# Optimization experiments

Hardware: AMD Instinct MI355X
Metric: run time of the kernel (lower is better)

The kernel has to match this reference:

```python
import jax, jax.numpy as jnp
import numpy as np

B, N, D, K, DSPACE, NFREQ = 4, 4096, 256, 16, 3, 5
BN_EPS = 1e-5


def setup_inputs() -> dict:
    key = jax.random.key(0)
    ks = jax.random.split(key, 12)
    s = 1.0 / np.sqrt(D)
    pe_in = DSPACE * 2 * NFREQ + DSPACE  # 33
    return {
        "xyz": jax.random.normal(ks[0], (B, N, DSPACE), jnp.float32),
        "feats": jax.random.normal(ks[1], (B, N, D), jnp.float32),
        "w_q": jax.random.uniform(ks[2], (D, D), jnp.float32, -s, s),
        "w_k": jax.random.uniform(ks[3], (D, D), jnp.float32, -s, s),
        "w_v": jax.random.uniform(ks[4], (D, D), jnp.float32, -s, s),
        "g_w1": jax.random.uniform(ks[5], (D, D), jnp.float32, -s, s),
        "g_b1": jax.random.uniform(ks[6], (D,), jnp.float32, -s, s),
        "g_w2": jax.random.uniform(ks[7], (D, D), jnp.float32, -s, s),
        "g_b2": jax.random.uniform(ks[8], (D,), jnp.float32, -s, s),
        "pe_w": jax.random.uniform(ks[9], (D, pe_in), jnp.float32, -s, s),
        "pe_b": jax.random.uniform(ks[10], (D,), jnp.float32, -s, s),
        "bn_w": jnp.ones((D,), jnp.float32),
        "bn_b": jnp.zeros((D,), jnp.float32),
    }


def _gather_knn(points, idx):
    # points [b,n,c], idx [b,n,k] -> [b,n,k,c]
    return jax.vmap(lambda p, i: p[i])(points, idx)


def reference(xyz, feats, w_q, w_k, w_v, g_w1, g_b1, g_w2, g_b2, pe_w, pe_b, bn_w, bn_b):
    # KNN (no grad in original): full pairwise sq-distance + top-k smallest
    dists = jnp.sum((xyz[:, :, None] - xyz[:, None]) ** 2, axis=-1)  # [b,n,n]
    _, knn_idx = jax.lax.top_k(-dists, K)  # [b,n,k], ascending distance
    knn_idx = jax.lax.stop_gradient(knn_idx)
    knn_xyz = jax.lax.stop_gradient(_gather_knn(xyz, knn_idx))  # [b,n,k,3]

    q = feats @ w_q.T                               # [b,n,d]
    k_g = _gather_knn(feats @ w_k.T, knn_idx)       # [b,n,k,d]
    v_g = _gather_knn(feats @ w_v.T, knn_idx)       # [b,n,k,d]

    pos_diff = xyz[:, :, None] - knn_xyz            # [b,n,k,3]
    freqs = jnp.linspace(1.0, 2.0 ** NFREQ, NFREQ).astype(pos_diff.dtype)
    embeds = [pos_diff]
    for f in freqs:
        embeds.append(jnp.sin(pos_diff * f))
        embeds.append(jnp.cos(pos_diff * f))
    pos_embed = jnp.concatenate(embeds, axis=-1)    # [b,n,k,33]
    pos_encode = pos_embed @ pe_w.T + pe_b          # [b,n,k,d]

    edges = q[:, :, None] - k_g + pos_encode        # [b,n,k,d]
    h = jax.nn.relu(edges @ g_w1.T + g_b1)
    attn = h @ g_w2.T + g_b2                        # [b,n,k,d]
    attn = jax.nn.softmax(attn, axis=-2)            # softmax over neighbors

    res = jnp.einsum('bnkf,bnkf->bnf', attn, v_g + pos_encode) + feats

    # BatchNorm1d over channel dim, training-mode batch stats (biased var)
    mean = jnp.mean(res, axis=(0, 1))
    var = jnp.var(res, axis=(0, 1))
    res = (res - mean) * jax.lax.rsqrt(var + BN_EPS) * bn_w + bn_b
    return res
```

## Files before the change

kernel.cpp:

```cpp
#include <hip/hip_runtime.h>

#define BB 4
#define NN 4096
#define DD 256
#define KK 16
#define PTS 2
#define SA 280
#define SE 104
#define SK 264

typedef __bf16 bf16;
typedef __attribute__((ext_vector_type(8))) __bf16 bf16x8;
typedef __attribute__((ext_vector_type(4))) __bf16 bf16x4;
typedef __attribute__((ext_vector_type(4))) float f32x4;

__global__ __launch_bounds__(256) void prep_kernel(
    const float* __restrict__ wq, const float* __restrict__ wk,
    const float* __restrict__ wv, const float* __restrict__ w1,
    const float* __restrict__ w2, const float* __restrict__ pw,
    bf16* __restrict__ wqb, bf16* __restrict__ wkb, bf16* __restrict__ wvb,
    bf16* __restrict__ w1b, bf16* __restrict__ w2b, bf16* __restrict__ pwb,
    float* __restrict__ sums) {
  const int idx = blockIdx.x * 256 + threadIdx.x;
  wqb[idx] = (bf16)wq[idx];
  wkb[idx] = (bf16)wk[idx];
  wvb[idx] = (bf16)wv[idx];
  w1b[idx] = (bf16)w1[idx];
  w2b[idx] = (bf16)w2[idx];
  if (idx < 256 * 64) {
    const int n = idx >> 6, c = idx & 63;
    pwb[idx] = (c < 33) ? (bf16)pw[n * 33 + c] : (bf16)0.f;
  }
  if (idx < 2 * DD) sums[idx] = 0.f;
}

__global__ __launch_bounds__(256, 2) void knn_v3(const float* __restrict__ xyz,
                                                 int* __restrict__ knn) {
  const int lane = threadIdx.x & 63;
  const int wv = threadIdx.x >> 6;
  const int row = blockIdx.x * 4 + wv;
  const int b = row >> 12, i = row & (NN - 1);
  const float* xb = xyz + (size_t)b * NN * 3;
  const float xi = xb[i * 3 + 0], yi = xb[i * 3 + 1], zi = xb[i * 3 + 2];
  unsigned long long cand[64];
#pragma unroll
  for (int c = 0; c < 64; ++c) {
    const int j = c * 64 + lane;
    const float dx = xi - xb[j * 3 + 0];
    const float dy = yi - xb[j * 3 + 1];
    const float dz = zi - xb[j * 3 + 2];
    const float d = dx * dx + dy * dy + dz * dz;
    const unsigned long long fb = (unsigned long long)(__float_as_uint(d)) + 1ull;
    cand[c] = (fb << 32) | (unsigned int)j;
  }
  unsigned long long gm[8];
#pragma unroll
  for (int g = 0; g < 8; ++g) {
    unsigned long long mn = cand[g * 8];
#pragma unroll
    for (int s = 1; s < 8; ++s)
      if (cand[g * 8 + s] < mn) mn = cand[g * 8 + s];
    gm[g] = mn;
  }
  unsigned int myj = 0u;
  for (int r = 0; r < KK; ++r) {
    unsigned long long lmin = gm[0];
#pragma unroll
    for (int g = 1; g < 8; ++g)
      if (gm[g] < lmin) lmin = gm[g];
#pragma unroll
    for (int off = 1; off < 64; off <<= 1) {
      const unsigned long long o = __shfl_xor(lmin, off);
      if (o < lmin) lmin = o;
    }
    if (lane == r) myj = (unsigned int)lmin;
#pragma unroll
    for (int g = 0; g < 8; ++g) {
      if (__ballot(gm[g] == lmin)) {
        unsigned long long nm = ~0ull;
#pragma unroll
        for (int s = 0; s < 8; ++s) {
          const unsigned long long v = cand[g * 8 + s];
          if (v > lmin && v < nm) nm = v;
        }
        if (gm[g] == lmin) gm[g] = nm;
      }
    }
  }
  if (lane < KK) knn[row * KK + lane] = (int)myj;
}

__global__ __launch_bounds__(256, 4) void proj_mfma(
    const float* __restrict__ feats, const bf16* __restrict__ wqb,
    const bf16* __restrict__ wkb, const bf16* __restrict__ wvb,
    bf16* __restrict__ qb, bf16* __restrict__ kfb, bf16* __restrict__ vfb) {
  const int t = threadIdx.x;
  const int lane = t & 63, wv = t >> 6;
  const int m = lane & 15, qd = lane >> 4;
  const size_t r0 = (size_t)blockIdx.x * 16;
  __shared__ __align__(16) bf16 fs[16][SA];
  const float4* f4 = (const float4*)(feats + r0 * DD);
#pragma unroll
  for (int i = 0; i < 4; ++i) {
    const int e = i * 256 + t;
    const float4 v = f4[e];
    bf16x4 w;
    w[0] = (bf16)v.x; w[1] = (bf16)v.y; w[2] = (bf16)v.z; w[3] = (bf16)v.w;
    *(bf16x4*)&fs[e >> 6][(e & 63) * 4] = w;
  }
  __syncthreads();
  bf16x8 afrag[8];
#pragma unroll
  for (int f = 0; f < 8; ++f)
    afrag[f] = *(const bf16x8*)&fs[m][f * 32 + qd * 8];
  const bf16* wmat[3] = {wqb, wkb, wvb};
  bf16* omat[3] = {qb, kfb, vfb};
  for (int mat = 0; mat < 3; ++mat) {
    const bf16* wb = wmat[mat];
    for (int nt = 0; nt < 4; ++nt) {
      const int n = wv * 64 + nt * 16 + m;
      bf16x8 bfr[8];
#pragma unroll
      for (int f = 0; f < 8; ++f)
        bfr[f] = *(const bf16x8*)(wb + (size_t)n * DD + f * 32 + qd * 8);
      f32x4 c = {0.f, 0.f, 0.f, 0.f};
#pragma unroll
      for (int f = 0; f < 8; ++f)
        c = __builtin_amdgcn_mfma_f32_16x16x32_bf16(afrag[f], bfr[f], c, 0, 0, 0);
#pragma unroll
      for (int rr = 0; rr < 4; ++rr)
        omat[mat][(r0 + qd * 4 + rr) * DD + n] = (bf16)c[rr];
    }
  }
}

__global__ __launch_bounds__(256, 3) void edge_v6(
    const float* __restrict__ xyz, const float* __restrict__ feats,
    const bf16* __restrict__ qb, const bf16* __restrict__ kfb,
    const bf16* __restrict__ vfb, const int* __restrict__ knn,
    const bf16* __restrict__ w1b, const float* __restrict__ g_b1,
    const bf16* __restrict__ w2b, const float* __restrict__ g_b2,
    const bf16* __restrict__ pwb, const float* __restrict__ pe_b,
    float* __restrict__ res) {
  const int t = threadIdx.x;
  const int lane = t & 63;
  const int wv = t >> 6;
  const int m = lane & 15;
  const int qd = lane >> 4;
  const int row0 = blockIdx.x * PTS;
  const int b = row0 >> 12;

  __shared__ __align__(16) bf16 bufA[PTS][16][SA];
  __shared__ __align__(16) char un_s[PTS * 16 * SA * 2];
  bf16(*bufB)[16][SA] = (bf16(*)[16][SA])un_s;
  bf16(*emb_s)[16][SE] = (bf16(*)[16][SE])un_s;
  __shared__ __align__(16) bf16 kf_s[PTS][16][SK];
  __shared__ int js_s[PTS][16];

  if (t < PTS * 16) js_s[t >> 4][t & 15] = knn[(row0 + (t >> 4)) * KK + (t & 15)];
  __syncthreads();

#pragma unroll
  for (int i = 0; i < 4; ++i) {
    const int e = i * 256 + t;
    const int p = e >> 9, rem = e & 511;
    const int k = rem >> 5, ch = rem & 31;
    const bf16x8 v =
        *(const bf16x8*)(kfb + ((size_t)(b * NN + js_s[p][k])) * DD + ch * 8);
    *(bf16x8*)&kf_s[p][k][ch * 8] = v;
  }

  const float* xb = xyz + (size_t)b * NN * 3;
  {
    const int k = t >> 4;
    const int c0 = (t & 15) * 6;
#pragma unroll
    for (int p = 0; p < PTS; ++p) {
      const int i = (row0 + p) & (NN - 1);
      const int j = js_s[p][k];
#pragma unroll
      for (int cc = 0; cc < 6; ++cc) {
        const int c = c0 + cc;
        float val = 0.f;
        if (c < 33) {
          const int ax = (c < 3) ? c : (c - 3) % 3;
          const float pd = xb[i * 3 + ax] - xb[j * 3 + ax];
          if (c < 3) {
            val = pd;
          } else {
            const int f = (c - 3) / 6;
            const float x = pd * fmaf(7.75f, (float)f, 1.0f);
            val = (((c - 3) % 6) < 3) ? __sinf(x) : __cosf(x);
          }
        }
        emb_s[p][k][c] = (bf16)val;
      }
    }
  }
  __syncthreads();

  float vpe[4][PTS][4];
  bf16x8 ea0[PTS], ea1[PTS];
#pragma unroll
  for (int p = 0; p < PTS; ++p) {
    ea0[p] = *(const bf16x8*)&emb_s[p][m][qd * 8];
    ea1[p] = *(const bf16x8*)&emb_s[p][m][32 + qd * 8];
  }
#pragma unroll
  for (int tt = 0; tt < 4; ++tt) {
    const int n = wv * 64 + tt * 16 + m;
    const bf16x8 b0 = *(const bf16x8*)(pwb + (size_t)n * 64 + qd * 8);
    const bf16x8 b1 = *(const bf16x8*)(pwb + (size_t)n * 64 + 32 + qd * 8);
    const float bias = pe_b[n];
#pragma unroll
    for (int p = 0; p < PTS; ++p) {
      f32x4 c = {bias, bias, bias, bias};
      c = __builtin_amdgcn_mfma_f32_16x16x32_bf16(ea0[p], b0, c, 0, 0, 0);
      c = __builtin_amdgcn_mfma_f32_16x16x32_bf16(ea1[p], b1, c, 0, 0, 0);
      const float qv = (float)qb[(size_t)(row0 + p) * DD + n];
#pragma unroll
      for (int rr = 0; rr < 4; ++rr) {
        const int krow = qd * 4 + rr;
        const size_t jr = ((size_t)(b * NN + js_s[p][krow])) * DD + n;
        bufA[p][krow][n] = (bf16)(qv - (float)kf_s[p][krow][n] + c[rr]);
        vpe[tt][p][rr] = (float)vfb[jr] + c[rr];
      }
    }
  }
  __syncthreads();

  {
    bf16x8 afrag[PTS][8];
#pragma unroll
    for (int p = 0; p < PTS; ++p)
#pragma unroll
      for (int f = 0; f < 8; ++f)
        afrag[p][f] = *(const bf16x8*)&bufA[p][m][f * 32 + qd * 8];
    for (int tt = 0; tt < 4; ++tt) {
      const int n = wv * 64 + tt * 16 + m;
      bf16x8 bfr[8];
#pragma unroll
      for (int f = 0; f < 8; ++f)
        bfr[f] = *(const bf16x8*)(w1b + (size_t)n * DD + f * 32 + qd * 8);
      const float bias = g_b1[n];
#pragma unroll
      for (int p = 0; p < PTS; ++p) {
        f32x4 c = {bias, bias, bias, bias};
#pragma unroll
        for (int f = 0; f < 8; ++f)
          c = __builtin_amdgcn_mfma_f32_16x16x32_bf16(afrag[p][f], bfr[f], c, 0, 0, 0);
#pragma unroll
        for (int rr = 0; rr < 4; ++rr)
          bufB[p][qd * 4 + rr][n] = (bf16)fmaxf(c[rr], 0.f);
      }
    }
  }
  __syncthreads();

  {
    bf16x8 afrag[PTS][8];
#pragma unroll
    for (int p = 0; p < PTS; ++p)
#pragma unroll
      for (int f = 0; f < 8; ++f)
        afrag[p][f] = *(const bf16x8*)&bufB[p][m][f * 32 + qd * 8];
#pragma unroll
    for (int tt = 0; tt < 4; ++tt) {
      const int n = wv * 64 + tt * 16 + m;
      bf16x8 bfr[8];
#pragma unroll
      for (int f = 0; f < 8; ++f)
        bfr[f] = *(const bf16x8*)(w2b + (size_t)n * DD + f * 32 + qd * 8);
      const float bias = g_b2[n];
#pragma unroll
      for (int p = 0; p < PTS; ++p) {
        f32x4 c = {bias, bias, bias, bias};
#pragma unroll
        for (int f = 0; f < 8; ++f)
          c = __builtin_amdgcn_mfma_f32_16x16x32_bf16(afrag[p][f], bfr[f], c, 0, 0, 0);
        float mx = fmaxf(fmaxf(c[0], c[1]), fmaxf(c[2], c[3]));
        mx = fmaxf(mx, __shfl_xor(mx, 16));
        mx = fmaxf(mx, __shfl_xor(mx, 32));
        float e[4], den = 0.f;
#pragma unroll
        for (int rr = 0; rr < 4; ++rr) {
          e[rr] = __expf(c[rr] - mx);
          den += e[rr];
        }
        den += __shfl_xor(den, 16);
        den += __shfl_xor(den, 32);
        float num = 0.f;
#pragma unroll
        for (int rr = 0; rr < 4; ++rr) num += e[rr] * vpe[tt][p][rr];
        num += __shfl_xor(num, 16);
        num += __shfl_xor(num, 32);
        if (qd == 0) {
          const size_t o = (size_t)(row0 + p) * DD + n;
          res[o] = num / den + feats[o];
        }
      }
    }
  }
}

__global__ __launch_bounds__(256) void bn_stats(const float* __restrict__ res,
                                                float* __restrict__ sums,
                                                float* __restrict__ sumsq) {
  const int t = threadIdx.x;
  const size_t r0 = (size_t)blockIdx.x * 32;
  float s = 0.f, s2 = 0.f;
  for (int r = 0; r < 32; ++r) {
    const float v = res[(r0 + r) * DD + t];
    s += v;
    s2 += v * v;
  }
  atomicAdd(&sums[t], s);
  atomicAdd(&sumsq[t], s2);
}

__global__ __launch_bounds__(256) void bn_apply(float* __restrict__ out,
                                                const float* __restrict__ sums,
                                                const float* __restrict__ sumsq,
                                                const float* __restrict__ bn_w,
                                                const float* __restrict__ bn_b) {
  const int idx = blockIdx.x * 256 + threadIdx.x;
  const int c = idx & (DD - 1);
  const float inv_n = 1.f / (float)(BB * NN);
  const float mean = sums[c] * inv_n;
  const float var = sumsq[c] * inv_n - mean * mean;
  const float v = out[idx];
  out[idx] = (v - mean) * rsqrtf(var + 1e-5f) * bn_w[c] + bn_b[c];
}

extern "C" void kernel_launch(void* const* d_in, const int* in_sizes, int n_in,
                              void* d_out, int out_size, void* d_ws,
                              size_t ws_size, hipStream_t stream) {
  (void)in_sizes; (void)n_in; (void)out_size; (void)ws_size;
  const float* xyz = (const float*)d_in[0];
  const float* feats = (const float*)d_in[1];
  const float* w_q = (const float*)d_in[2];
  const float* w_k = (const float*)d_in[3];
  const float* w_v = (const float*)d_in[4];
  const float* g_w1 = (const float*)d_in[5];
  const float* g_b1 = (const float*)d_in[6];
  const float* g_w2 = (const float*)d_in[7];
  const float* g_b2 = (const float*)d_in[8];
  const float* pe_w = (const float*)d_in[9];
  const float* pe_b = (const float*)d_in[10];
  const float* bn_w = (const float*)d_in[11];
  const float* bn_b = (const float*)d_in[12];
  float* out = (float*)d_out;

  const int BN = BB * NN;
  char* w = (char*)d_ws;
  int* knn = (int*)w;       w += (size_t)BN * KK * 4;
  bf16* qb = (bf16*)w;      w += (size_t)BN * DD * 2;
  bf16* kfb = (bf16*)w;     w += (size_t)BN * DD * 2;
  bf16* vfb = (bf16*)w;     w += (size_t)BN * DD * 2;
  float* sums = (float*)w;  w += DD * 4;
  float* sumsq = (float*)w; w += DD * 4;
  bf16* wqb = (bf16*)w;     w += (size_t)DD * DD * 2;
  bf16* wkb = (bf16*)w;     w += (size_t)DD * DD * 2;
  bf16* wvb = (bf16*)w;     w += (size_t)DD * DD * 2;
  bf16* w1b = (bf16*)w;     w += (size_t)DD * DD * 2;
  bf16* w2b = (bf16*)w;     w += (size_t)DD * DD * 2;
  bf16* pwb = (bf16*)w;     w += (size_t)DD * 64 * 2;

  prep_kernel<<<DD * DD / 256, 256, 0, stream>>>(w_q, w_k, w_v, g_w1, g_w2,
                                                 pe_w, wqb, wkb, wvb, w1b, w2b,
                                                 pwb, sums);
  knn_v3<<<BN / 4, 256, 0, stream>>>(xyz, knn);
  proj_mfma<<<BN / 16, 256, 0, stream>>>(feats, wqb, wkb, wvb, qb, kfb, vfb);
  edge_v6<<<BN / PTS, 256, 0, stream>>>(xyz, feats, qb, kfb, vfb, knn, w1b,
                                        g_b1, w2b, g_b2, pwb, pe_b, out);
  bn_stats<<<BN / 32, 256, 0, stream>>>(out, sums, sumsq);
  bn_apply<<<BN, 256, 0, stream>>>(out, sums, sumsq, bn_w, bn_b);
}
```

Baseline: 645.0 us.

## Merge prep, KNN and projection kernels; fuse BN stats into edge kernel

Prep, KNN and Q/K/V projection now run as one launch, with the block index choosing the role, so the independent KNN and projection work can overlap and fewer kernels are launched. The projection converts the fp32 weights to bf16 inline, so the separate bf16 copies of w_q, w_k and w_v are no longer needed. The edge kernel reads gathered K values straight from global memory instead of staging them in LDS, which frees shared memory. It also accumulates per-channel BatchNorm sums with atomics, which removes the separate stats pass. In exchange, each block reconverts the weights redundantly, there are many more atomics, and the merged kernel uses a single launch bound, 2, for roles that differ in register use.

```diff
diff --git a/kernel.cpp b/kernel.cpp
--- a/kernel.cpp
+++ b/kernel.cpp
@@ -7,141 +7,145 @@
 #define PTS 2
 #define SA 280
 #define SE 104
-#define SK 264
 
 typedef __bf16 bf16;
 typedef __attribute__((ext_vector_type(8))) __bf16 bf16x8;
 typedef __attribute__((ext_vector_type(4))) __bf16 bf16x4;
 typedef __attribute__((ext_vector_type(4))) float f32x4;
 
-__global__ __launch_bounds__(256) void prep_kernel(
-    const float* __restrict__ wq, const float* __restrict__ wk,
-    const float* __restrict__ wv, const float* __restrict__ w1,
-    const float* __restrict__ w2, const float* __restrict__ pw,
-    bf16* __restrict__ wqb, bf16* __restrict__ wkb, bf16* __restrict__ wvb,
-    bf16* __restrict__ w1b, bf16* __restrict__ w2b, bf16* __restrict__ pwb,
-    float* __restrict__ sums) {
-  const int idx = blockIdx.x * 256 + threadIdx.x;
-  wqb[idx] = (bf16)wq[idx];
-  wkb[idx] = (bf16)wk[idx];
-  wvb[idx] = (bf16)wv[idx];
-  w1b[idx] = (bf16)w1[idx];
-  w2b[idx] = (bf16)w2[idx];
-  if (idx < 256 * 64) {
-    const int n = idx >> 6, c = idx & 63;
-    pwb[idx] = (c < 33) ? (bf16)pw[n * 33 + c] : (bf16)0.f;
-  }
-  if (idx < 2 * DD) sums[idx] = 0.f;
+__global__ __launch_bounds__(256, 2) void setup_kernel(
+    const float* __restrict__ xyz, const float* __restrict__ feats,
+    const float* __restrict__ w_q, const float* __restrict__ w_k,
+    const float* __restrict__ w_v, const float* __restrict__ g_w1,
+    const float* __restrict__ g_w2, const float* __restrict__ pe_w,
+    int* __restrict__ knn, bf16* __restrict__ qb, bf16* __restrict__ kfb,
+    bf16* __restrict__ vfb, bf16* __restrict__ w1b, bf16* __restrict__ w2b,
+    bf16* __restrict__ pwb, float* __restrict__ sums) {
+  const int bid = blockIdx.x;
+  const int t = threadIdx.x;
+  __shared__ __align__(16) bf16 fs[16][SA];
+
+  if (bid < 256) {
+    const int idx = bid * 256 + t;
+    w1b[idx] = (bf16)g_w1[idx];
+    w2b[idx] = (bf16)g_w2[idx];
+    if (idx < 256 * 64) {
+      const int n = idx >> 6, c = idx & 63;
+      pwb[idx] = (c < 33) ? (bf16)pe_w[n * 33 + c] : (bf16)0.f;
+    }
+    if (idx < 2 * DD) sums[idx] = 0.f;
+    return;
+  }
+  if (bid < 256 + 4096) {
+    const int lane = t & 63;
+    const int row = (bid - 256) * 4 + (t >> 6);
+    const int b = row >> 12, i = row & (NN - 1);
+    const float* xb = xyz + (size_t)b * NN * 3;
+    const float xi = xb[i * 3 + 0], yi = xb[i * 3 + 1], zi = xb[i * 3 + 2];
+    unsigned long long cand[64];
+#pragma unroll
+    for (int c = 0; c < 64; ++c) {
+      const int j = c * 64 + lane;
+      const float dx = xi - xb[j * 3 + 0];
+      const float dy = yi - xb[j * 3 + 1];
+      const float dz = zi - xb[j * 3 + 2];
+      const float d = dx * dx + dy * dy + dz * dz;
+      const unsigned long long fb =
+          (unsigned long long)(__float_as_uint(d)) + 1ull;
+      cand[c] = (fb << 32) | (unsigned int)j;
+    }
+    unsigned long long gm[8];
+#pragma unroll
+    for (int g = 0; g < 8; ++g) {
+      unsigned long long mn = cand[g * 8];
+#pragma unroll
+      for (int s = 1; s < 8; ++s)
+        if (cand[g * 8 + s] < mn) mn = cand[g * 8 + s];
+      gm[g] = mn;
+    }
+    unsigned int myj = 0u;
+    for (int r = 0; r < KK; ++r) {
+      unsigned long long lmin = gm[0];
+#pragma unroll
+      for (int g = 1; g < 8; ++g)
+        if (gm[g] < lmin) lmin = gm[g];
+#pragma unroll
+      for (int off = 1; off < 64; off <<= 1) {
+        const unsigned long long o = __shfl_xor(lmin, off);
+        if (o < lmin) lmin = o;
+      }
+      if (lane == r) myj = (unsigned int)lmin;
+#pragma unroll
+      for (int g = 0; g < 8; ++g) {
+        if (__ballot(gm[g] == lmin)) {
+          unsigned long long nm = ~0ull;
+#pragma unroll
+          for (int s = 0; s < 8; ++s) {
+            const unsigned long long v = cand[g * 8 + s];
+            if (v > lmin && v < nm) nm = v;
+          }
+          if (gm[g] == lmin) gm[g] = nm;
+        }
+      }
+    }
+    if (lane < KK) knn[row * KK + lane] = (int)myj;
+    return;
+  }
+  {
+    const int lane = t & 63, wv = t >> 6;
+    const int m = lane & 15, qd = lane >> 4;
+    const size_t r0 = (size_t)(bid - (256 + 4096)) * 16;
+    const float4* f4 = (const float4*)(feats + r0 * DD);
+#pragma unroll
+    for (int i = 0; i < 4; ++i) {
+      const int e = i * 256 + t;
+      const float4 v = f4[e];
+      bf16x4 w;
+      w[0] = (bf16)v.x; w[1] = (bf16)v.y; w[2] = (bf16)v.z; w[3] = (bf16)v.w;
+      *(bf16x4*)&fs[e >> 6][(e & 63) * 4] = w;
+    }
+    __syncthreads();
+    bf16x8 afrag[8];
+#pragma unroll
+    for (int f = 0; f < 8; ++f)
+      afrag[f] = *(const bf16x8*)&fs[m][f * 32 + qd * 8];
+    const float* wmat[3] = {w_q, w_k, w_v};
+    bf16* omat[3] = {qb, kfb, vfb};
+    for (int mat = 0; mat < 3; ++mat) {
+      const float* wb = wmat[mat];
+      for (int nt = 0; nt < 4; ++nt) {
+        const int n = wv * 64 + nt * 16 + m;
+        bf16x8 bfr[8];
+#pragma unroll
+        for (int f = 0; f < 8; ++f) {
+          const float4 wa = *(const float4*)(wb + (size_t)n * DD + f * 32 + qd * 8);
+          const float4 wc = *(const float4*)(wb + (size_t)n * DD + f * 32 + qd * 8 + 4);
+          bf16x8 x;
+          x[0] = (bf16)wa.x; x[1] = (bf16)wa.y; x[2] = (bf16)wa.z; x[3] = (bf16)wa.w;
+          x[4] = (bf16)wc.x; x[5] = (bf16)wc.y; x[6] = (bf16)wc.z; x[7] = (bf16)wc.w;
+          bfr[f] = x;
+        }
+        f32x4 c = {0.f, 0.f, 0.f, 0.f};
+#pragma unroll
+        for (int f = 0; f < 8; ++f)
+          c = __builtin_amdgcn_mfma_f32_16x16x32_bf16(afrag[f], bfr[f], c, 0, 0, 0);
+#pragma unroll
+        for (int rr = 0; rr < 4; ++rr)
+          omat[mat][(r0 + qd * 4 + rr) * DD + n] = (bf16)c[rr];
+      }
+    }
+  }
 }
 
-__global__ __launch_bounds__(256, 2) void knn_v3(const float* __restrict__ xyz,
-                                                 int* __restrict__ knn) {
-  const int lane = threadIdx.x & 63;
-  const int wv = threadIdx.x >> 6;
-  const int row = blockIdx.x * 4 + wv;
-  const int b = row >> 12, i = row & (NN - 1);
-  const float* xb = xyz + (size_t)b * NN * 3;
-  const float xi = xb[i * 3 + 0], yi = xb[i * 3 + 1], zi = xb[i * 3 + 2];
-  unsigned long long cand[64];
-#pragma unroll
-  for (int c = 0; c < 64; ++c) {
-    const int j = c * 64 + lane;
-    const float dx = xi - xb[j * 3 + 0];
-    const float dy = yi - xb[j * 3 + 1];
-    const float dz = zi - xb[j * 3 + 2];
-    const float d = dx * dx + dy * dy + dz * dz;
-    const unsigned long long fb = (unsigned long long)(__float_as_uint(d)) + 1ull;
-    cand[c] = (fb << 32) | (unsigned int)j;
-  }
-  unsigned long long gm[8];
-#pragma unroll
-  for (int g = 0; g < 8; ++g) {
-    unsigned long long mn = cand[g * 8];
-#pragma unroll
-    for (int s = 1; s < 8; ++s)
-      if (cand[g * 8 + s] < mn) mn = cand[g * 8 + s];
-    gm[g] = mn;
-  }
-  unsigned int myj = 0u;
-  for (int r = 0; r < KK; ++r) {
-    unsigned long long lmin = gm[0];
-#pragma unroll
-    for (int g = 1; g < 8; ++g)
-      if (gm[g] < lmin) lmin = gm[g];
-#pragma unroll
-    for (int off = 1; off < 64; off <<= 1) {
-      const unsigned long long o = __shfl_xor(lmin, off);
-      if (o < lmin) lmin = o;
-    }
-    if (lane == r) myj = (unsigned int)lmin;
-#pragma unroll
-    for (int g = 0; g < 8; ++g) {
-      if (__ballot(gm[g] == lmin)) {
-        unsigned long long nm = ~0ull;
-#pragma unroll
-        for (int s = 0; s < 8; ++s) {
-          const unsigned long long v = cand[g * 8 + s];
-          if (v > lmin && v < nm) nm = v;
-        }
-        if (gm[g] == lmin) gm[g] = nm;
-      }
-    }
-  }
-  if (lane < KK) knn[row * KK + lane] = (int)myj;
-}
-
-__global__ __launch_bounds__(256, 4) void proj_mfma(
-    const float* __restrict__ feats, const bf16* __restrict__ wqb,
-    const bf16* __restrict__ wkb, const bf16* __restrict__ wvb,
-    bf16* __restrict__ qb, bf16* __restrict__ kfb, bf16* __restrict__ vfb) {
-  const int t = threadIdx.x;
-  const int lane = t & 63, wv = t >> 6;
-  const int m = lane & 15, qd = lane >> 4;
-  const size_t r0 = (size_t)blockIdx.x * 16;
-  __shared__ __align__(16) bf16 fs[16][SA];
-  const float4* f4 = (const float4*)(feats + r0 * DD);
-#pragma unroll
-  for (int i = 0; i < 4; ++i) {
-    const int e = i * 256 + t;
-    const float4 v = f4[e];
-    bf16x4 w;
-    w[0] = (bf16)v.x; w[1] = (bf16)v.y; w[2] = (bf16)v.z; w[3] = (bf16)v.w;
-    *(bf16x4*)&fs[e >> 6][(e & 63) * 4] = w;
-  }
-  __syncthreads();
-  bf16x8 afrag[8];
-#pragma unroll
-  for (int f = 0; f < 8; ++f)
-    afrag[f] = *(const bf16x8*)&fs[m][f * 32 + qd * 8];
-  const bf16* wmat[3] = {wqb, wkb, wvb};
-  bf16* omat[3] = {qb, kfb, vfb};
-  for (int mat = 0; mat < 3; ++mat) {
-    const bf16* wb = wmat[mat];
-    for (int nt = 0; nt < 4; ++nt) {
-      const int n = wv * 64 + nt * 16 + m;
-      bf16x8 bfr[8];
-#pragma unroll
-      for (int f = 0; f < 8; ++f)
-        bfr[f] = *(const bf16x8*)(wb + (size_t)n * DD + f * 32 + qd * 8);
-      f32x4 c = {0.f, 0.f, 0.f, 0.f};
-#pragma unroll
-      for (int f = 0; f < 8; ++f)
-        c = __builtin_amdgcn_mfma_f32_16x16x32_bf16(afrag[f], bfr[f], c, 0, 0, 0);
-#pragma unroll
-      for (int rr = 0; rr < 4; ++rr)
-        omat[mat][(r0 + qd * 4 + rr) * DD + n] = (bf16)c[rr];
-    }
-  }
-}
-
-__global__ __launch_bounds__(256, 3) void edge_v6(
+__global__ __launch_bounds__(256, 3) void edge_v7(
     const float* __restrict__ xyz, const float* __restrict__ feats,
     const bf16* __restrict__ qb, const bf16* __restrict__ kfb,
     const bf16* __restrict__ vfb, const int* __restrict__ knn,
     const bf16* __restrict__ w1b, const float* __restrict__ g_b1,
     const bf16* __restrict__ w2b, const float* __restrict__ g_b2,
     const bf16* __restrict__ pwb, const float* __restrict__ pe_b,
-    float* __restrict__ res) {
+    float* __restrict__ res, float* __restrict__ sums,
+    float* __restrict__ sumsq) {
   const int t = threadIdx.x;
   const int lane = t & 63;
   const int wv = t >> 6;
@@ -154,21 +158,10 @@
   __shared__ __align__(16) char un_s[PTS * 16 * SA * 2];
   bf16(*bufB)[16][SA] = (bf16(*)[16][SA])un_s;
   bf16(*emb_s)[16][SE] = (bf16(*)[16][SE])un_s;
-  __shared__ __align__(16) bf16 kf_s[PTS][16][SK];
   __shared__ int js_s[PTS][16];
 
   if (t < PTS * 16) js_s[t >> 4][t & 15] = knn[(row0 + (t >> 4)) * KK + (t & 15)];
   __syncthreads();
-
-#pragma unroll
-  for (int i = 0; i < 4; ++i) {
-    const int e = i * 256 + t;
-    const int p = e >> 9, rem = e & 511;
-    const int k = rem >> 5, ch = rem & 31;
-    const bf16x8 v =
-        *(const bf16x8*)(kfb + ((size_t)(b * NN + js_s[p][k])) * DD + ch * 8);
-    *(bf16x8*)&kf_s[p][k][ch * 8] = v;
-  }
 
   const float* xb = xyz + (size_t)b * NN * 3;
   {
@@ -222,7 +215,7 @@
       for (int rr = 0; rr < 4; ++rr) {
         const int krow = qd * 4 + rr;
         const size_t jr = ((size_t)(b * NN + js_s[p][krow])) * DD + n;
-        bufA[p][krow][n] = (bf16)(qv - (float)kf_s[p][krow][n] + c[rr]);
+        bufA[p][krow][n] = (bf16)(qv - (float)kfb[jr] + c[rr]);
         vpe[tt][p][rr] = (float)vfb[jr] + c[rr];
       }
     }
@@ -272,6 +265,7 @@
       for (int f = 0; f < 8; ++f)
         bfr[f] = *(const bf16x8*)(w2b + (size_t)n * DD + f * 32 + qd * 8);
       const float bias = g_b2[n];
+      float bs = 0.f, bs2 = 0.f;
 #pragma unroll
       for (int p = 0; p < PTS; ++p) {
         f32x4 c = {bias, bias, bias, bias};
@@ -296,26 +290,18 @@
         num += __shfl_xor(num, 32);
         if (qd == 0) {
           const size_t o = (size_t)(row0 + p) * DD + n;
-          res[o] = num / den + feats[o];
-        }
-      }
-    }
-  }
-}
-
-__global__ __launch_bounds__(256) void bn_stats(const float* __restrict__ res,
-                                                float* __restrict__ sums,
-                                                float* __restrict__ sumsq) {
-  const int t = threadIdx.x;
-  const size_t r0 = (size_t)blockIdx.x * 32;
-  float s = 0.f, s2 = 0.f;
-  for (int r = 0; r < 32; ++r) {
-    const float v = res[(r0 + r) * DD + t];
-    s += v;
-    s2 += v * v;
-  }
-  atomicAdd(&sums[t], s);
-  atomicAdd(&sumsq[t], s2);
+          const float out = num / den + feats[o];
+          res[o] = out;
+          bs += out;
+          bs2 += out * out;
+        }
+      }
+      if (qd == 0) {
+        atomicAdd(&sums[n], bs);
+        atomicAdd(&sumsq[n], bs2);
+      }
+    }
+  }
 }
 
 __global__ __launch_bounds__(256) void bn_apply(float* __restrict__ out,
@@ -359,20 +345,15 @@
   bf16* vfb = (bf16*)w;     w += (size_t)BN * DD * 2;
   float* sums = (float*)w;  w += DD * 4;
   float* sumsq = (float*)w; w += DD * 4;
-  bf16* wqb = (bf16*)w;     w += (size_t)DD * DD * 2;
-  bf16* wkb = (bf16*)w;     w += (size_t)DD * DD * 2;
-  bf16* wvb = (bf16*)w;     w += (size_t)DD * DD * 2;
   bf16* w1b = (bf16*)w;     w += (size_t)DD * DD * 2;
   bf16* w2b = (bf16*)w;     w += (size_t)DD * DD * 2;
   bf16* pwb = (bf16*)w;     w += (size_t)DD * 64 * 2;
 
-  prep_kernel<<<DD * DD / 256, 256, 0, stream>>>(w_q, w_k, w_v, g_w1, g_w2,
-                                                 pe_w, wqb, wkb, wvb, w1b, w2b,
-                                                 pwb, sums);
-  knn_v3<<<BN / 4, 256, 0, stream>>>(xyz, knn);
-  proj_mfma<<<BN / 16, 256, 0, stream>>>(feats, wqb, wkb, wvb, qb, kfb, vfb);
-  edge_v6<<<BN / PTS, 256, 0, stream>>>(xyz, feats, qb, kfb, vfb, knn, w1b,
-                                        g_b1, w2b, g_b2, pwb, pe_b, out);
-  bn_stats<<<BN / 32, 256, 0, stream>>>(out, sums, sumsq);
+  setup_kernel<<<256 + 4096 + 1024, 256, 0, stream>>>(
+      xyz, feats, w_q, w_k, w_v, g_w1, g_w2, pe_w, knn, qb, kfb, vfb, w1b, w2b,
+      pwb, sums);
+  edge_v7<<<BN / PTS, 256, 0, stream>>>(xyz, feats, qb, kfb, vfb, knn, w1b,
+                                        g_b1, w2b, g_b2, pwb, pe_b, out, sums,
+                                        sumsq);
   bn_apply<<<BN, 256, 0, stream>>>(out, sums, sumsq, bn_w, bn_b);
 }
```

Result: no change. 648.5 us (+0.6%).
